# Optimization experiments

Measured on AMD Instinct MI355X. Metric: run time of the kernel, lower is better.

## Reference

```python
import jax, jax.numpy as jnp
import numpy as np

C = 128; D_INNER = 256; D_STATE = 16; D_CONV = 4; DT_RANK = 8; SCALE_MLP = 2


def layernorm(x, g, b, eps=1e-5):
    m = x.mean(-1, keepdims=True)
    v = ((x - m) ** 2).mean(-1, keepdims=True)
    return (x - m) * jax.lax.rsqrt(v + eps) * g + b


def causal_conv(x, w, b):
    # x: (B, L, D); w: (D, K) depthwise causal conv; b: (D,)
    K = w.shape[1]
    xt = x.transpose(0, 2, 1)  # (B, D, L)
    out = jax.lax.conv_general_dilated(
        xt, w[:, None, :], (1,), [(K - 1, 0)],
        dimension_numbers=("NCH", "OIH", "NCH"), feature_group_count=w.shape[0])
    return (out + b[None, :, None]).transpose(0, 2, 1)


def selective_scan(u, delta, A, Bm, Cm, Dv):
    # u, delta: (B, L, D); A: (D, N); Bm, Cm: (B, L, N); Dv: (D,)
    def step(h, inp):
        u_t, d_t, B_t, C_t = inp  # (B,D),(B,D),(B,N),(B,N)
        dA = jnp.exp(d_t[..., None] * A)                      # (B, D, N)
        h = dA * h + (d_t * u_t)[..., None] * B_t[:, None, :]  # (B, D, N)
        y = jnp.einsum("bdn,bn->bd", h, C_t)
        return h, y
    Bsz, L, Din = u.shape
    h0 = jnp.zeros((Bsz, Din, A.shape[1]), u.dtype)
    inputs = (u.transpose(1, 0, 2), delta.transpose(1, 0, 2),
              Bm.transpose(1, 0, 2), Cm.transpose(1, 0, 2))
    _, ys = jax.lax.scan(step, h0, inputs)
    return ys.transpose(1, 0, 2) + u * Dv


def mamba_branch(xc, z, cw, cb, Wx_, Wdt_, bdt_, Al, Dv):
    u = jax.nn.silu(causal_conv(xc, cw, cb))
    xdbl = u @ Wx_.T  # (B, L, dt_rank + 2*d_state)
    dr = Wdt_.shape[1]; ds = Al.shape[1]
    dt = jax.nn.softplus(xdbl[..., :dr] @ Wdt_.T + bdt_)
    Bm = xdbl[..., dr:dr + ds]
    Cm = xdbl[..., dr + ds:]
    y = selective_scan(u, dt, -jnp.exp(Al), Bm, Cm, Dv)
    return y * jax.nn.silu(z)


def setup_inputs():
    key = jax.random.key(0)
    ks = jax.random.split(key, 20)
    w = lambda k, shape, s=0.02: jax.random.normal(k, shape, jnp.float32) * s
    A_log = jnp.log(jnp.tile(jnp.arange(1, D_STATE + 1, dtype=jnp.float32), (D_INNER, 1)))
    dt_bias = jnp.full((D_INNER,), jnp.log(jnp.expm1(0.01)), jnp.float32)
    return dict(
        x=jax.random.normal(ks[0], (4, 256, 64, C), jnp.float32),
        g1=jnp.ones((C,), jnp.float32), b1=jnp.zeros((C,), jnp.float32),
        W_in=w(ks[1], (2 * D_INNER, C)),
        conv_w=w(ks[2], (D_INNER, D_CONV), 0.2), conv_b=jnp.zeros((D_INNER,), jnp.float32),
        Wx=w(ks[3], (DT_RANK + 2 * D_STATE, D_INNER)),
        Wdt=w(ks[4], (D_INNER, DT_RANK), 0.1), bdt=dt_bias,
        A_log=A_log, D=jnp.ones((D_INNER,), jnp.float32),
        conv_wb=w(ks[5], (D_INNER, D_CONV), 0.2), conv_bb=jnp.zeros((D_INNER,), jnp.float32),
        Wxb=w(ks[6], (DT_RANK + 2 * D_STATE, D_INNER)),
        Wdtb=w(ks[7], (D_INNER, DT_RANK), 0.1), bdtb=dt_bias,
        A_b_log=A_log, D_b=jnp.ones((D_INNER,), jnp.float32),
        W_out=w(ks[8], (C, D_INNER)),
        g2=jnp.ones((C,), jnp.float32), b2=jnp.zeros((C,), jnp.float32),
        g3=jnp.ones((C,), jnp.float32), b3=jnp.zeros((C,), jnp.float32),
        W1m=w(ks[9], (C, SCALE_MLP * C)), b1m=jnp.zeros((SCALE_MLP * C,), jnp.float32),
        W2m=w(ks[10], (SCALE_MLP * C, C)), b2m=jnp.zeros((C,), jnp.float32),
    )


def reference(x, g1, b1, W_in, conv_w, conv_b, Wx, Wdt, bdt, A_log, D,
              conv_wb, conv_bb, Wxb, Wdtb, bdtb, A_b_log, D_b, W_out,
              g2, b2, g3, b3, W1m, b1m, W2m, b2m):
    B, T, N, Cc = x.shape
    xs = x.transpose(0, 2, 1, 3).reshape(B * N, T, Cc)
    # --- CustomBiMamba: LN -> (Dropout eval=identity) -> BiMamba v2 -> LN, residual ---
    h = layernorm(xs, g1, b1)
    xz = h @ W_in.T  # (B*N, T, 2*d_inner)
    xc, z = jnp.split(xz, 2, axis=-1)
    y_f = mamba_branch(xc, z, conv_w, conv_b, Wx, Wdt, bdt, A_log, D)
    y_b = mamba_branch(xc[:, ::-1], z[:, ::-1], conv_wb, conv_bb, Wxb, Wdtb, bdtb,
                       A_b_log, D_b)[:, ::-1]
    y = (y_f + y_b) @ W_out.T
    y = layernorm(y, g2, b2)
    xs = y + xs
    xo = xs.reshape(B, N, T, Cc).transpose(0, 2, 1, 3)
    # --- MLP residual ---
    h2 = layernorm(xo, g3, b3)
    mlp = jax.nn.gelu(h2 @ W1m + b1m, approximate=False) @ W2m + b2m
    return xo + mlp
```

## Files before the change

### kernel.cpp

```cpp
#include <hip/hip_runtime.h>
#include <hip/hip_bf16.h>
#include <math.h>

#define CC 128
#define DI 256
#define SSEQ 256
#define ROWS 65536

typedef __hip_bfloat16 bf16;
typedef __attribute__((ext_vector_type(8))) short short8;
typedef __attribute__((ext_vector_type(4))) float float4v;
typedef __attribute__((ext_vector_type(2))) float f32x2;

__device__ __forceinline__ float to_f(float v) { return v; }
__device__ __forceinline__ float to_f(bf16 v)  { return __bfloat162float(v); }
__device__ __forceinline__ bf16  f2b(float v)  { return __float2bfloat16(v); }
__device__ __forceinline__ float bf2f_bits(short v) {
    union { unsigned u; float f; } c; c.u = ((unsigned)(unsigned short)v) << 16; return c.f;
}
__device__ __forceinline__ f32x2 mk2(float a, float b) { f32x2 r; r.x = a; r.y = b; return r; }
__device__ __forceinline__ f32x2 fma2(f32x2 a, f32x2 b, f32x2 c) { return a * b + c; }

__device__ __forceinline__ float wave_sum(float v) {
    #pragma unroll
    for (int o = 1; o < 64; o <<= 1) v += __shfl_xor(v, o, 64);
    return v;
}
__device__ __forceinline__ float silu_f(float x) {
    return x * __builtin_amdgcn_rcpf(1.f + __expf(-x));
}
__device__ __forceinline__ float gelu_f(float x) { return 0.5f * x * (1.f + erff(x * 0.70710678118654752f)); }
__device__ __forceinline__ float softplus_f(float x) {
    return (x > 20.f) ? x : __logf(1.f + __expf(x));
}

__global__ __launch_bounds__(256) void ln1_kernel(const float* __restrict__ x,
                                                  const float* __restrict__ g,
                                                  const float* __restrict__ b,
                                                  bf16* __restrict__ out) {
    int wave = threadIdx.x >> 6, lane = threadIdx.x & 63;
    int r = blockIdx.x * 4 + wave;
    int s = r >> 8, t = r & 255;
    int bb = s >> 6, n = s & 63;
    size_t xbase = (((size_t)(bb * 256 + t)) * 64 + n) * CC;
    float v0 = x[xbase + lane], v1 = x[xbase + lane + 64];
    float s1 = wave_sum(v0 + v1);
    float s2 = wave_sum(v0 * v0 + v1 * v1);
    float m = s1 * (1.f / 128.f);
    float var = s2 * (1.f / 128.f) - m * m;
    float rstd = rsqrtf(var + 1e-5f);
    size_t ob = (size_t)r * CC;
    out[ob + lane]      = f2b((v0 - m) * rstd * g[lane]      + b[lane]);
    out[ob + lane + 64] = f2b((v1 - m) * rstd * g[lane + 64] + b[lane + 64]);
}

__global__ __launch_bounds__(256) void ln3_kernel(const float* __restrict__ in,
                                                  const float* __restrict__ g,
                                                  const float* __restrict__ b,
                                                  bf16* __restrict__ out) {
    int wave = threadIdx.x >> 6, lane = threadIdx.x & 63;
    int r = blockIdx.x * 4 + wave;
    size_t ib = (size_t)r * CC;
    float v0 = in[ib + lane], v1 = in[ib + lane + 64];
    float s1 = wave_sum(v0 + v1);
    float s2 = wave_sum(v0 * v0 + v1 * v1);
    float m = s1 * (1.f / 128.f);
    float var = s2 * (1.f / 128.f) - m * m;
    float rstd = rsqrtf(var + 1e-5f);
    out[ib + lane]      = f2b((v0 - m) * rstd * g[lane]      + b[lane]);
    out[ib + lane + 64] = f2b((v1 - m) * rstd * g[lane + 64] + b[lane + 64]);
}

template <bool BTR, int EPI, int KTILES>
__global__ __launch_bounds__(256) void mfma_gemm_kernel(const bf16* __restrict__ A, int lda,
                                                        const float* __restrict__ B,
                                                        const float* __restrict__ bias,
                                                        void* __restrict__ Cout, int ldc,
                                                        int N, int K) {
    __shared__ bf16 As[64][40];
    __shared__ bf16 Bs[64][40];
    int tid = threadIdx.x;
    int m0 = blockIdx.x * 64;
    int n0 = blockIdx.y * 64;
    int wv = tid >> 6, lane = tid & 63;
    int lrow = lane & 15, quad = lane >> 4;
    int lk = quad * 8;
    float4v acc[4] = {};
    #pragma unroll
    for (int kt = 0; kt < KTILES; kt++) {
        int k0 = kt * 32;
        {
            int m = tid >> 2, part = tid & 3;
            uint4 v = *(const uint4*)(A + (size_t)(m0 + m) * lda + k0 + part * 8);
            *(uint4*)&As[m][part * 8] = v;
        }
        if (BTR) {
            int n = tid >> 2, part = tid & 3;
            const float* src = B + (size_t)(n0 + n) * K + k0 + part * 8;
            bf16 tmp[8];
            #pragma unroll
            for (int j = 0; j < 8; j++) tmp[j] = f2b(src[j]);
            *(uint4*)&Bs[n][part * 8] = *(uint4*)tmp;
        } else {
            int kk = tid >> 3, nf = (tid & 7) * 8;
            const float* src = B + (size_t)(k0 + kk) * N + n0 + nf;
            #pragma unroll
            for (int j = 0; j < 8; j++) Bs[nf + j][kk] = f2b(src[j]);
        }
        __syncthreads();
        short8 a = *(const short8*)&As[wv * 16 + lrow][lk];
        #pragma unroll
        for (int jt = 0; jt < 4; jt++) {
            short8 bfr = *(const short8*)&Bs[jt * 16 + lrow][lk];
            acc[jt] = __builtin_amdgcn_mfma_f32_16x16x32_bf16(a, bfr, acc[jt], 0, 0, 0);
        }
        __syncthreads();
    }
    #pragma unroll
    for (int jt = 0; jt < 4; jt++) {
        int col = n0 + jt * 16 + lrow;
        float bs = (EPI >= 1) ? bias[col] : 0.f;
        #pragma unroll
        for (int r = 0; r < 4; r++) {
            int row = m0 + wv * 16 + quad * 4 + r;
            float v = acc[jt][r] + bs;
            if (EPI == 1) v = gelu_f(v);
            if (EPI == 2) {
                float* Cf = (float*)Cout;
                Cf[(size_t)row * ldc + col] += v;
            } else {
                bf16* Cb = (bf16*)Cout;
                Cb[(size_t)row * ldc + col] = f2b(v);
            }
        }
    }
}

__global__ __launch_bounds__(256) void mfma_ln2res_kernel(const bf16* __restrict__ YF,
                                                          const bf16* __restrict__ YB,
                                                          const bf16* __restrict__ xz,
                                                          const float* __restrict__ Wout,
                                                          const float* __restrict__ g,
                                                          const float* __restrict__ b,
                                                          const float* __restrict__ x,
                                                          float* __restrict__ out) {
    __shared__ bf16 As[64][40];
    __shared__ bf16 Bs[128][40];
    int tid = threadIdx.x;
    int m0 = blockIdx.x * 64;
    int wv = tid >> 6, lane = tid & 63;
    int lrow = lane & 15, quad = lane >> 4;
    int lk = quad * 8;
    float4v acc[8] = {};
    #pragma unroll
    for (int kt = 0; kt < 8; kt++) {
        int k0 = kt * 32;
        {
            int m = tid >> 2, part = tid & 3;
            size_t off = (size_t)(m0 + m) * 256 + k0 + part * 8;
            short8 vf = *(const short8*)(YF + off);
            short8 vb = *(const short8*)(YB + off);
            short8 vz = *(const short8*)(xz + (size_t)(m0 + m) * 512 + 256 + k0 + part * 8);
            bf16 tmp[8];
            #pragma unroll
            for (int j = 0; j < 8; j++)
                tmp[j] = f2b((bf2f_bits(vf[j]) + bf2f_bits(vb[j])) * silu_f(bf2f_bits(vz[j])));
            *(uint4*)&As[m][part * 8] = *(uint4*)tmp;
        }
        #pragma unroll
        for (int it = 0; it < 2; it++) {
            int idx = tid + it * 256;
            int n = idx >> 2, part = idx & 3;
            const float* src = Wout + (size_t)n * 256 + k0 + part * 8;
            bf16 tmp[8];
            #pragma unroll
            for (int j = 0; j < 8; j++) tmp[j] = f2b(src[j]);
            *(uint4*)&Bs[n][part * 8] = *(uint4*)tmp;
        }
        __syncthreads();
        short8 a = *(const short8*)&As[wv * 16 + lrow][lk];
        #pragma unroll
        for (int jt = 0; jt < 8; jt++) {
            short8 bfr = *(const short8*)&Bs[jt * 16 + lrow][lk];
            acc[jt] = __builtin_amdgcn_mfma_f32_16x16x32_bf16(a, bfr, acc[jt], 0, 0, 0);
        }
        __syncthreads();
    }
    #pragma unroll
    for (int r = 0; r < 4; r++) {
        float ps = 0.f, ps2 = 0.f;
        #pragma unroll
        for (int jt = 0; jt < 8; jt++) { float v = acc[jt][r]; ps += v; ps2 += v * v; }
        #pragma unroll
        for (int o = 1; o < 16; o <<= 1) {
            ps  += __shfl_xor(ps, o, 64);
            ps2 += __shfl_xor(ps2, o, 64);
        }
        float m = ps * (1.f / 128.f);
        float var = ps2 * (1.f / 128.f) - m * m;
        float rstd = rsqrtf(var + 1e-5f);
        int row = m0 + wv * 16 + quad * 4 + r;
        int s = row >> 8, t = row & 255;
        int bb = s >> 6, n = s & 63;
        size_t xbase = (((size_t)(bb * 256 + t)) * 64 + n) * CC;
        #pragma unroll
        for (int jt = 0; jt < 8; jt++) {
            int col = jt * 16 + lrow;
            out[xbase + col] = (acc[jt][r] - m) * rstd * g[col] + b[col] + x[xbase + col];
        }
    }
}

template <int DIR>
__global__ __launch_bounds__(256) void mfma_conv_kernel(const bf16* __restrict__ xz,
                                                        const float* __restrict__ cw,
                                                        const float* __restrict__ cb,
                                                        const float* __restrict__ Wx,
                                                        bf16* __restrict__ C,
                                                        bf16* __restrict__ U) {
    __shared__ bf16 As[64][40];
    __shared__ bf16 Bs[48][40];
    int tid = threadIdx.x;
    int s = blockIdx.x >> 2;
    int t0 = (blockIdx.x & 3) * 64;
    int wv = tid >> 6, lane = tid & 63;
    int lrow = lane & 15, quad = lane >> 4;
    int lk = quad * 8;
    float4v acc[3] = {};
    #pragma unroll
    for (int kt = 0; kt < 8; kt++) {
        int k0 = kt * 32;
        {
            int m = tid >> 2, part = tid & 3;
            int t = t0 + m;
            int dbase = k0 + part * 8;
            float a[8];
            float4 w4[8];
            #pragma unroll
            for (int i = 0; i < 8; i++) {
                a[i]  = cb[dbase + i];
                w4[i] = ((const float4*)cw)[dbase + i];
            }
            #pragma unroll
            for (int j = 0; j < 4; j++) {
                int tj = t - 3 + j;
                if (tj >= 0) {
                    int src = DIR ? (255 - tj) : tj;
                    uint4 v = *(const uint4*)(xz + (size_t)(s * 256 + src) * 512 + dbase);
                    short8 sv = *(short8*)&v;
                    #pragma unroll
                    for (int i = 0; i < 8; i++) {
                        float w = (j == 0) ? w4[i].x : (j == 1) ? w4[i].y : (j == 2) ? w4[i].z : w4[i].w;
                        a[i] += w * bf2f_bits(sv[i]);
                    }
                }
            }
            bf16 tmp[8];
            #pragma unroll
            for (int i = 0; i < 8; i++) tmp[i] = f2b(silu_f(a[i]));
            *(uint4*)&As[m][part * 8] = *(uint4*)tmp;
            int tu = DIR ? (255 - t) : t;
            *(uint4*)&U[((size_t)(s * 256 + tu)) * 256 + dbase] = *(uint4*)tmp;
        }
        {
            int n = tid >> 2, part = tid & 3;
            if (n < 48) {
                bf16 tmp[8];
                #pragma unroll
                for (int j = 0; j < 8; j++)
                    tmp[j] = (n < 40) ? f2b(Wx[(size_t)n * 256 + k0 + part * 8 + j]) : f2b(0.f);
                *(uint4*)&Bs[n][part * 8] = *(uint4*)tmp;
            }
        }
        __syncthreads();
        short8 a = *(const short8*)&As[wv * 16 + lrow][lk];
        #pragma unroll
        for (int jt = 0; jt < 3; jt++) {
            short8 bfr = *(const short8*)&Bs[jt * 16 + lrow][lk];
            acc[jt] = __builtin_amdgcn_mfma_f32_16x16x32_bf16(a, bfr, acc[jt], 0, 0, 0);
        }
        __syncthreads();
    }
    #pragma unroll
    for (int jt = 0; jt < 3; jt++) {
        int col = jt * 16 + lrow;
        if (col < 40) {
            #pragma unroll
            for (int r = 0; r < 4; r++) {
                int row = t0 + wv * 16 + quad * 4 + r;
                C[(size_t)(s * 256 + row) * 40 + col] = f2b(acc[jt][r]);
            }
        }
    }
}


#define LOADROW(R, T) do {                                                  \
    const float4* rp_ = (const float4*)(rows + (T) * 40);                   \
    R##0 = rp_[0]; R##1 = rp_[1]; R##2 = rp_[2]; R##3 = rp_[3];             \
    R##4 = rp_[4]; R##5 = rp_[5]; R##6 = rp_[6]; R##7 = rp_[7];             \
    R##8 = rp_[8]; R##9 = rp_[9];                                           \
} while (0)

#define SCAN_STEP(JJ, R) do {                                               \
    float u_ = to_f(ub[(JJ) * 256 + d]);                                    \
    f32x2 acc2 = mk2((R##0).x, (R##0).y) * wdt01;                           \
    acc2 = fma2(mk2((R##0).z, (R##0).w), wdt23, acc2);                      \
    acc2 = fma2(mk2((R##1).x, (R##1).y), wdt45, acc2);                      \
    acc2 = fma2(mk2((R##1).z, (R##1).w), wdt67, acc2);                      \
    float dtr_ = bd + acc2.x + acc2.y;                                      \
    float dt_ = softplus_f(dtr_);                                           \
    float du_ = dt_ * u_;                                                   \
    float d1 = __expf(dt_ * A0);                                            \
    float d2v = d1 * d1;                                                    \
    f32x2 pw0 = mk2(d1, d2v);                                               \
    f32x2 dd2 = mk2(d2v, d2v);                                              \
    f32x2 pw1 = pw0 * dd2, pw2 = pw1 * dd2, pw3 = pw2 * dd2;                \
    f32x2 dd8 = mk2(pw3.y, pw3.y);                                          \
    f32x2 pw4 = pw0 * dd8, pw5 = pw1 * dd8, pw6 = pw2 * dd8, pw7 = pw3 * dd8; \
    f32x2 du2 = mk2(du_, du_);                                              \
    hp0 = fma2(pw0, hp0, du2 * mk2((R##2).x, (R##2).y));                    \
    hp1 = fma2(pw1, hp1, du2 * mk2((R##2).z, (R##2).w));                    \
    hp2 = fma2(pw2, hp2, du2 * mk2((R##3).x, (R##3).y));                    \
    hp3 = fma2(pw3, hp3, du2 * mk2((R##3).z, (R##3).w));                    \
    hp4 = fma2(pw4, hp4, du2 * mk2((R##4).x, (R##4).y));                    \
    hp5 = fma2(pw5, hp5, du2 * mk2((R##4).z, (R##4).w));                    \
    hp6 = fma2(pw6, hp6, du2 * mk2((R##5).x, (R##5).y));                    \
    hp7 = fma2(pw7, hp7, du2 * mk2((R##5).z, (R##5).w));                    \
    f32x2 ya = hp0 * mk2((R##6).x, (R##6).y);                               \
    f32x2 yb2 = hp1 * mk2((R##6).z, (R##6).w);                              \
    ya = fma2(hp2, mk2((R##7).x, (R##7).y), ya);                            \
    yb2 = fma2(hp3, mk2((R##7).z, (R##7).w), yb2);                          \
    ya = fma2(hp4, mk2((R##8).x, (R##8).y), ya);                            \
    yb2 = fma2(hp5, mk2((R##8).z, (R##8).w), yb2);                          \
    ya = fma2(hp6, mk2((R##9).x, (R##9).y), ya);                            \
    yb2 = fma2(hp7, mk2((R##9).z, (R##9).w), yb2);                          \
    f32x2 ys = ya + yb2;                                                    \
    float yv_ = ys.x + ys.y + u_ * Dd;                                      \
    *yp = f2b(yv_); yp += ystep;                                            \
} while (0)

#define STAGE_U(BUF, C0) do {                                               \
    _Pragma("unroll")                                                       \
    for (int q_ = 0; q_ < 4; q_++) {                                        \
        int flat_ = q_ * 256 + tid;                                         \
        int j_ = flat_ >> 5, w_ = flat_ & 31;                               \
        int t_ = (C0) + j_;                                                 \
        int grow_ = dir ? (255 - t_) : t_;                                  \
        ((uint4*)u_lds)[(BUF) * 1024 + flat_] =                             \
            *((const uint4*)(Y + ((size_t)(s * 256 + grow_)) * 256) + w_);  \
    }                                                                       \
} while (0)

__global__ __launch_bounds__(256, 2) void scan_kernel(
        const bf16* __restrict__ xdbl_f, const bf16* __restrict__ xdbl_b,
        const float* __restrict__ Wdt_f, const float* __restrict__ bdt_f,
        const float* __restrict__ Alog_f, const float* __restrict__ D_f,
        const float* __restrict__ Wdt_b, const float* __restrict__ bdt_b,
        const float* __restrict__ Alog_b, const float* __restrict__ D_b,
        bf16* __restrict__ YF, bf16* __restrict__ YB) {
    __shared__ float rows[256 * 40];
    __shared__ bf16  u_lds[2 * 8192];
    int tid = threadIdx.x;
    int dir = blockIdx.x >> 8;
    int s = blockIdx.x & 255;
    int d = tid;

    const bf16* xd = (dir ? xdbl_b : xdbl_f) + (size_t)s * 10240;
    #pragma unroll
    for (int i = 0; i < 5; i++) {
        int idx = i * 256 + tid;
        uint4 v = ((const uint4*)xd)[idx];
        short8 sv = *(short8*)&v;
        float f[8];
        #pragma unroll
        for (int j = 0; j < 8; j++) f[j] = bf2f_bits(sv[j]);
        *(float4*)&rows[idx * 8]     = *(float4*)&f[0];
        *(float4*)&rows[idx * 8 + 4] = *(float4*)&f[4];
    }

    const float* Alog = dir ? Alog_b : Alog_f;
    const float* Wdtp = dir ? Wdt_b  : Wdt_f;
    float Aarr[16];
    #pragma unroll
    for (int n = 0; n < 16; n++) Aarr[n] = -__expf(Alog[d * 16 + n]);
    f32x2 wdt01 = mk2(Wdtp[d * 8 + 0], Wdtp[d * 8 + 1]);
    f32x2 wdt23 = mk2(Wdtp[d * 8 + 2], Wdtp[d * 8 + 3]);
    f32x2 wdt45 = mk2(Wdtp[d * 8 + 4], Wdtp[d * 8 + 5]);
    f32x2 wdt67 = mk2(Wdtp[d * 8 + 6], Wdtp[d * 8 + 7]);
    float bd = dir ? bdt_b[d] : bdt_f[d];
    float Dd = dir ? D_b[d]   : D_f[d];
    bf16* Y = dir ? YB : YF;

    float A0 = Aarr[0];
    int pw = 1;
    #pragma unroll
    for (int n = 1; n < 16; n++)
        pw &= (fabsf(Aarr[n] - (float)(n + 1) * A0) <= 1e-4f * fabsf(Aarr[n]) + 1e-6f) ? 1 : 0;
    pw = __all(pw);

    STAGE_U(0, 0);
    __syncthreads();

    bf16* yp = Y + ((size_t)(s * 256 + (dir ? 255 : 0))) * 256 + d;
    ptrdiff_t ystep = dir ? -256 : 256;

    if (pw) {
        f32x2 hp0 = {}, hp1 = {}, hp2 = {}, hp3 = {},
              hp4 = {}, hp5 = {}, hp6 = {}, hp7 = {};
        float4 ra0, ra1, ra2, ra3, ra4, ra5, ra6, ra7, ra8, ra9;
        float4 rb0, rb1, rb2, rb3, rb4, rb5, rb6, rb7, rb8, rb9;
        LOADROW(ra, 0);
        #pragma unroll 1
        for (int c = 0; c < 8; c++) {
            if (c + 1 < 8) STAGE_U((c + 1) & 1, (c + 1) * 32);
            const bf16* ub = u_lds + (c & 1) * 8192;
            int tc = c * 32;
            #pragma unroll 2
            for (int j = 0; j < 32; j += 2) {
                int t = tc + j;
                LOADROW(rb, t + 1);
                SCAN_STEP(j, ra);
                if (t + 2 < 256) LOADROW(ra, t + 2);
                SCAN_STEP(j + 1, rb);
            }
            __syncthreads();
        }
    } else {
        float h[16];
        #pragma unroll
        for (int n = 0; n < 16; n++) h[n] = 0.f;
        #pragma unroll 1
        for (int c = 0; c < 8; c++) {
            if (c + 1 < 8) STAGE_U((c + 1) & 1, (c + 1) * 32);
            const bf16* ub = u_lds + (c & 1) * 8192;
            int tc = c * 32;
            #pragma unroll 1
            for (int j = 0; j < 32; j++) {
                float u = to_f(ub[j * 256 + d]);
                const float* row = rows + (tc + j) * 40;
                float4 q0 = *(const float4*)(row);
                float4 q1 = *(const float4*)(row + 4);
                float dtr = bd;
                dtr += q0.x * wdt01.x + q0.y * wdt01.y + q0.z * wdt23.x + q0.w * wdt23.y;
                dtr += q1.x * wdt45.x + q1.y * wdt45.y + q1.z * wdt67.x + q1.w * wdt67.y;
                float dt = softplus_f(dtr);
                float du = dt * u, y = 0.f;
                #pragma unroll
                for (int n = 0; n < 16; n++) {
                    float dA = __expf(dt * Aarr[n]);
                    h[n] = dA * h[n] + du * row[8 + n];
                    y += h[n] * row[24 + n];
                }
                y += u * Dd;
                *yp = f2b(y); yp += ystep;
            }
            __syncthreads();
        }
    }
}

extern "C" void kernel_launch(void* const* d_in, const int* in_sizes, int n_in,
                              void* d_out, int out_size, void* d_ws, size_t ws_size,
                              hipStream_t stream) {
    const float* x      = (const float*)d_in[0];
    const float* g1     = (const float*)d_in[1];
    const float* b1     = (const float*)d_in[2];
    const float* W_in   = (const float*)d_in[3];
    const float* conv_w = (const float*)d_in[4];
    const float* conv_b = (const float*)d_in[5];
    const float* Wx     = (const float*)d_in[6];
    const float* Wdt    = (const float*)d_in[7];
    const float* bdt    = (const float*)d_in[8];
    const float* A_log  = (const float*)d_in[9];
    const float* Dvec   = (const float*)d_in[10];
    const float* conv_wb= (const float*)d_in[11];
    const float* conv_bb= (const float*)d_in[12];
    const float* Wxb    = (const float*)d_in[13];
    const float* Wdtb   = (const float*)d_in[14];
    const float* bdtb   = (const float*)d_in[15];
    const float* A_b_log= (const float*)d_in[16];
    const float* D_b    = (const float*)d_in[17];
    const float* W_out  = (const float*)d_in[18];
    const float* g2     = (const float*)d_in[19];
    const float* b2     = (const float*)d_in[20];
    const float* g3     = (const float*)d_in[21];
    const float* b3     = (const float*)d_in[22];
    const float* W1m    = (const float*)d_in[23];
    const float* b1m    = (const float*)d_in[24];
    const float* W2m    = (const float*)d_in[25];
    const float* b2m    = (const float*)d_in[26];

    bf16* ws  = (bf16*)d_ws;
    bf16* XZ  = ws;
    bf16* YF  = ws + 33554432UL;
    bf16* YB  = ws + 50331648UL;
    bf16* H2  = ws;
    bf16* HID = ws + 8388608UL;
    float* out = (float*)d_out;
    bf16* LN1OUT = (bf16*)d_out;
    bf16* XDBL_F = (bf16*)d_out;
    bf16* XDBL_B = (bf16*)d_out + 2621440UL;

    ln1_kernel<<<ROWS / 4, 256, 0, stream>>>(x, g1, b1, LN1OUT);
    mfma_gemm_kernel<true, 0, 4><<<dim3(ROWS / 64, 8), 256, 0, stream>>>(
        LN1OUT, CC, W_in, nullptr, XZ, 512, 512, CC);
    mfma_conv_kernel<0><<<SSEQ * 4, 256, 0, stream>>>(XZ, conv_w, conv_b, Wx, XDBL_F, YF);
    mfma_conv_kernel<1><<<SSEQ * 4, 256, 0, stream>>>(XZ, conv_wb, conv_bb, Wxb, XDBL_B, YB);
    scan_kernel<<<512, 256, 0, stream>>>(XDBL_F, XDBL_B,
        Wdt, bdt, A_log, Dvec, Wdtb, bdtb, A_b_log, D_b, YF, YB);
    mfma_ln2res_kernel<<<ROWS / 64, 256, 0, stream>>>(YF, YB, XZ, W_out, g2, b2, x, out);
    ln3_kernel<<<ROWS / 4, 256, 0, stream>>>(out, g3, b3, H2);
    mfma_gemm_kernel<false, 1, 4><<<dim3(ROWS / 64, 4), 256, 0, stream>>>(
        H2, CC, W1m, b1m, HID, 2 * CC, 2 * CC, CC);
    mfma_gemm_kernel<false, 2, 8><<<dim3(ROWS / 64, 2), 256, 0, stream>>>(
        HID, 2 * CC, W2m, b2m, out, CC, CC, 2 * CC);
}
```

Before: 483.5 us.

## Fuse LN3, MLP up-projection with GELU, and down-projection into one kernel

Replaces the separate LN3 kernel and two MLP GEMM launches with one kernel per 64-row tile. It normalizes rows into shared memory, computes the 256-wide hidden activations with GELU into shared memory, then runs the second GEMM and adds the result into the output residual in place. This removes the bf16 round-trips through global memory for the LN output and the hidden activations, plus two launches. In exchange each block reloads and converts the full W1m/W2m weights from fp32, uses about 60KB of shared memory (limiting occupancy), and holds large accumulator arrays in registers.

```diff
diff --git a/kernel.cpp b/kernel.cpp
--- a/kernel.cpp
+++ b/kernel.cpp
@@ -52,23 +52,6 @@
     size_t ob = (size_t)r * CC;
     out[ob + lane]      = f2b((v0 - m) * rstd * g[lane]      + b[lane]);
     out[ob + lane + 64] = f2b((v1 - m) * rstd * g[lane + 64] + b[lane + 64]);
-}
-
-__global__ __launch_bounds__(256) void ln3_kernel(const float* __restrict__ in,
-                                                  const float* __restrict__ g,
-                                                  const float* __restrict__ b,
-                                                  bf16* __restrict__ out) {
-    int wave = threadIdx.x >> 6, lane = threadIdx.x & 63;
-    int r = blockIdx.x * 4 + wave;
-    size_t ib = (size_t)r * CC;
-    float v0 = in[ib + lane], v1 = in[ib + lane + 64];
-    float s1 = wave_sum(v0 + v1);
-    float s2 = wave_sum(v0 * v0 + v1 * v1);
-    float m = s1 * (1.f / 128.f);
-    float var = s2 * (1.f / 128.f) - m * m;
-    float rstd = rsqrtf(var + 1e-5f);
-    out[ib + lane]      = f2b((v0 - m) * rstd * g[lane]      + b[lane]);
-    out[ib + lane + 64] = f2b((v1 - m) * rstd * g[lane + 64] + b[lane + 64]);
 }
 
 template <bool BTR, int EPI, int KTILES>
@@ -460,6 +443,122 @@
     }
 }
 
+__global__ __launch_bounds__(256) void mlp_fused_kernel(
+        float* __restrict__ out,
+        const float* __restrict__ g3, const float* __restrict__ b3,
+        const float* __restrict__ W1m, const float* __restrict__ b1m,
+        const float* __restrict__ W2m, const float* __restrict__ b2m) {
+    __shared__ bf16 As[64][136];
+    __shared__ bf16 Hs[64][264];
+    __shared__ bf16 Bs[256][40];
+    int tid = threadIdx.x;
+    int m0 = blockIdx.x * 64;
+    int wv = tid >> 6, lane = tid & 63;
+    int lrow = lane & 15, quad = lane >> 4;
+    int lk = quad * 8;
+
+    {
+        int m = tid >> 2, part = tid & 3;
+        const float* src = out + (size_t)(m0 + m) * CC + part * 32;
+        float v[32];
+        #pragma unroll
+        for (int i = 0; i < 8; i++) {
+            float4 q = ((const float4*)src)[i];
+            v[i * 4 + 0] = q.x; v[i * 4 + 1] = q.y;
+            v[i * 4 + 2] = q.z; v[i * 4 + 3] = q.w;
+        }
+        float s1 = 0.f, s2 = 0.f;
+        #pragma unroll
+        for (int i = 0; i < 32; i++) { s1 += v[i]; s2 += v[i] * v[i]; }
+        s1 += __shfl_xor(s1, 1, 64); s2 += __shfl_xor(s2, 1, 64);
+        s1 += __shfl_xor(s1, 2, 64); s2 += __shfl_xor(s2, 2, 64);
+        float mean = s1 * (1.f / 128.f);
+        float var = s2 * (1.f / 128.f) - mean * mean;
+        float rstd = rsqrtf(var + 1e-5f);
+        #pragma unroll
+        for (int i8 = 0; i8 < 4; i8++) {
+            bf16 tmp[8];
+            #pragma unroll
+            for (int j = 0; j < 8; j++) {
+                int col = part * 32 + i8 * 8 + j;
+                tmp[j] = f2b((v[i8 * 8 + j] - mean) * rstd * g3[col] + b3[col]);
+            }
+            *(uint4*)&As[m][part * 32 + i8 * 8] = *(uint4*)tmp;
+        }
+    }
+    __syncthreads();
+
+    {
+        float4v acc1[16] = {};
+        #pragma unroll
+        for (int kt = 0; kt < 4; kt++) {
+            int k0 = kt * 32;
+            #pragma unroll
+            for (int it = 0; it < 4; it++) {
+                int idx = tid + it * 256;
+                int kk = idx >> 5;
+                int nf = (idx & 31) * 8;
+                const float* srcB = W1m + (size_t)(k0 + kk) * 256 + nf;
+                #pragma unroll
+                for (int j = 0; j < 8; j++) Bs[nf + j][kk] = f2b(srcB[j]);
+            }
+            __syncthreads();
+            short8 a = *(const short8*)&As[wv * 16 + lrow][k0 + lk];
+            #pragma unroll
+            for (int jt = 0; jt < 16; jt++) {
+                short8 bfr = *(const short8*)&Bs[jt * 16 + lrow][lk];
+                acc1[jt] = __builtin_amdgcn_mfma_f32_16x16x32_bf16(a, bfr, acc1[jt], 0, 0, 0);
+            }
+            __syncthreads();
+        }
+        #pragma unroll
+        for (int jt = 0; jt < 16; jt++) {
+            int col = jt * 16 + lrow;
+            float bs = b1m[col];
+            #pragma unroll
+            for (int r = 0; r < 4; r++) {
+                int row = wv * 16 + quad * 4 + r;
+                Hs[row][col] = f2b(gelu_f(acc1[jt][r] + bs));
+            }
+        }
+    }
+    __syncthreads();
+
+    float4v acc2[8] = {};
+    #pragma unroll
+    for (int kt = 0; kt < 8; kt++) {
+        int k0 = kt * 32;
+        #pragma unroll
+        for (int it = 0; it < 2; it++) {
+            int idx = tid + it * 256;
+            int kk = idx >> 4;
+            int nf = (idx & 15) * 8;
+            const float* srcB = W2m + (size_t)(k0 + kk) * 128 + nf;
+            #pragma unroll
+            for (int j = 0; j < 8; j++) Bs[nf + j][kk] = f2b(srcB[j]);
+        }
+        __syncthreads();
+        short8 a = *(const short8*)&Hs[wv * 16 + lrow][k0 + lk];
+        #pragma unroll
+        for (int jt = 0; jt < 8; jt++) {
+            short8 bfr = *(const short8*)&Bs[jt * 16 + lrow][lk];
+            acc2[jt] = __builtin_amdgcn_mfma_f32_16x16x32_bf16(a, bfr, acc2[jt], 0, 0, 0);
+        }
+        __syncthreads();
+    }
+    #pragma unroll
+    for (int jt = 0; jt < 8; jt++) {
+        int col = jt * 16 + lrow;
+        float bs = b2m[col];
+        #pragma unroll
+        for (int r = 0; r < 4; r++) {
+            int row = m0 + wv * 16 + quad * 4 + r;
+            float* p = out + (size_t)row * CC + col;
+            *p = *p + acc2[jt][r] + bs;
+        }
+    }
+}
+
 extern "C" void kernel_launch(void* const* d_in, const int* in_sizes, int n_in,
                               void* d_out, int out_size, void* d_ws, size_t ws_size,
                               hipStream_t stream) {
@@ -495,8 +594,6 @@
     bf16* XZ  = ws;
     bf16* YF  = ws + 33554432UL;
     bf16* YB  = ws + 50331648UL;
-    bf16* H2  = ws;
-    bf16* HID = ws + 8388608UL;
     float* out = (float*)d_out;
     bf16* LN1OUT = (bf16*)d_out;
     bf16* XDBL_F = (bf16*)d_out;
@@ -510,9 +607,5 @@
     scan_kernel<<<512, 256, 0, stream>>>(XDBL_F, XDBL_B,
         Wdt, bdt, A_log, Dvec, Wdtb, bdtb, A_b_log, D_b, YF, YB);
     mfma_ln2res_kernel<<<ROWS / 64, 256, 0, stream>>>(YF, YB, XZ, W_out, g2, b2, x, out);
-    ln3_kernel<<<ROWS / 4, 256, 0, stream>>>(out, g3, b3, H2);
-    mfma_gemm_kernel<false, 1, 4><<<dim3(ROWS / 64, 4), 256, 0, stream>>>(
-        H2, CC, W1m, b1m, HID, 2 * CC, 2 * CC, CC);
-    mfma_gemm_kernel<false, 2, 8><<<dim3(ROWS / 64, 2), 256, 0, stream>>>(
-        HID, 2 * CC, W2m, b2m, out, CC, CC, 2 * CC);
-}
+    mlp_fused_kernel<<<ROWS / 64, 256, 0, stream>>>(out, g3, b3, W1m, b1m, W2m, b2m);
+}
```

Measured after the change: 531.1 us. +9.8%, slower.
